# Optimization experiments

Hardware: AMD Instinct MI355X
Metric: run time of the kernel (lower is better)

Reference implementation:

```python
import jax, jax.numpy as jnp
import numpy as np

B, C, H, W = 4, 128, 64, 64


def setup_inputs() -> dict:
    key = jax.random.key(0)
    ks = jax.random.split(key, 8)
    return {
        "x": jax.random.normal(ks[0], (B, C, H, W), dtype=jnp.float32),
        "Wq": jax.random.normal(ks[1], (C // 4, C), dtype=jnp.float32) * 0.05,
        "bq": jax.random.normal(ks[2], (C // 4,), dtype=jnp.float32) * 0.05,
        "Wk": jax.random.normal(ks[3], (C // 4, C), dtype=jnp.float32) * 0.05,
        "bk": jax.random.normal(ks[4], (C // 4,), dtype=jnp.float32) * 0.05,
        "Wv": jax.random.normal(ks[5], (C, C), dtype=jnp.float32) * 0.05,
        "bv": jax.random.normal(ks[6], (C,), dtype=jnp.float32) * 0.05,
        "gamma": jnp.full((1,), 0.1, dtype=jnp.float32),
        "pos": jax.random.normal(ks[7], (1, C, 32, 32), dtype=jnp.float32) * 0.02,
    }


def reference(x, Wq, bq, Wk, bk, Wv, bv, gamma, pos):
    b, c, h, w = x.shape
    n = h * w
    # bilinear upsample of position encoding (half-pixel centers = torch align_corners=False)
    pe = jax.image.resize(pos, (1, c, h, w), method="bilinear")
    scale_factor = min(1.0, 16.0 / max(h, w))  # static shapes -> python float
    xp = x + scale_factor * 0.1 * pe
    # 1x1 conv projections as einsums; q/k: [b, c/4, n], v: [b, c, n]
    q = (jnp.einsum("bchw,oc->bohw", xp, Wq) + bq[None, :, None, None]).reshape(b, -1, n)
    k = (jnp.einsum("bchw,oc->bohw", xp, Wk) + bk[None, :, None, None]).reshape(b, -1, n)
    v = (jnp.einsum("bchw,oc->bohw", xp, Wv) + bv[None, :, None, None]).reshape(b, c, n)
    # scores[b, i, j] = <q_i, k_j> / (sqrt(C) + eps); softmax over j
    scores = jnp.einsum("bdn,bdm->bnm", q, k) / (c ** 0.5 + 1e-08)
    attn = jax.nn.softmax(scores, axis=-1)
    # out = V @ attn^T  -> [b, c, n]
    out = jnp.einsum("bcn,bmn->bcm", v, attn).reshape(b, c, h, w)
    return gamma[0] * out + xp
```

## Files before the change

kernel.cpp:

```cpp
#include <hip/hip_runtime.h>
#include <hip/hip_bf16.h>
#include <cstdint>
#include <cstddef>

typedef __attribute__((ext_vector_type(8))) short bf16x8;
typedef __attribute__((ext_vector_type(4))) float f32x4;
typedef __attribute__((ext_vector_type(16))) float f32x16;
typedef __attribute__((ext_vector_type(2))) unsigned int u32x2;
typedef unsigned int u32;
typedef unsigned short u16;
typedef unsigned char u8;

__device__ __forceinline__ u16 f2bf(float f) {
  union { float f; u32 u; } v; v.f = f;
  u32 r = v.u + 0x7FFFu + ((v.u >> 16) & 1u);
  return (u16)(r >> 16);
}
__device__ __forceinline__ u32 pk2(float a, float b) {
  return (u32)f2bf(a) | ((u32)f2bf(b) << 16);
}
__device__ __forceinline__ float bfhi(u32 u) {
  union { u32 u; float f; } v; v.u = u & 0xFFFF0000u; return v.f;
}
__device__ __forceinline__ float bflo(u32 u) {
  union { u32 u; float f; } v; v.u = u << 16; return v.f;
}
__device__ __forceinline__ float fexp2(float x) {
  return __builtin_amdgcn_exp2f(x);
}

__device__ __forceinline__ void proj_tile(int mts, int li, int g,
    const u16* tb, int tb_stride_u16, int n0, int b,
    const float* Wq, const float* bq, const float* Wk, const float* bk,
    const float* Wv, const float* bv,
    u8* q8, u8* k8, u8* v2) {
  const float qks = 0.35709468f;
  int row = mts * 16 + li;
  const float* wsrc = row < 32 ? Wq + (size_t)row * 128
                    : row < 64 ? Wk + (size_t)(row - 32) * 128
                               : Wv + (size_t)(row - 64) * 128;
  int ob = mts * 16 + g * 4;
  const float* bsrc = ob < 32 ? bq + ob : ob < 64 ? bk + (ob - 32) : bv + (ob - 64);
  f32x4 acc[4];
#pragma unroll
  for (int nt = 0; nt < 4; ++nt) acc[nt] = (f32x4){0.f, 0.f, 0.f, 0.f};
#pragma unroll
  for (int kc = 0; kc < 4; ++kc) {
    float4 wa = *(const float4*)(wsrc + kc * 32 + g * 8);
    float4 wb = *(const float4*)(wsrc + kc * 32 + g * 8 + 4);
    union { u32 u[4]; bf16x8 v; } af;
    af.u[0] = pk2(wa.x, wa.y); af.u[1] = pk2(wa.z, wa.w);
    af.u[2] = pk2(wb.x, wb.y); af.u[3] = pk2(wb.z, wb.w);
    bf16x8 bfr[4];
#pragma unroll
    for (int nt = 0; nt < 4; ++nt)
      bfr[nt] = *(const bf16x8*)(tb + (size_t)(nt * 16 + li) * tb_stride_u16 + kc * 32 + g * 8);
#pragma unroll
    for (int nt = 0; nt < 4; ++nt)
      acc[nt] = __builtin_amdgcn_mfma_f32_16x16x32_bf16(af.v, bfr[nt], acc[nt], 0, 0, 0);
  }
  float bias[4];
#pragma unroll
  for (int r = 0; r < 4; ++r) bias[r] = bsrc[r];
#pragma unroll
  for (int nt = 0; nt < 4; ++nt) {
    int n = n0 + nt * 16 + li;
    float v0 = acc[nt][0] + bias[0];
    float v1 = acc[nt][1] + bias[1];
    float v2v = acc[nt][2] + bias[2];
    float v3 = acc[nt][3] + bias[3];
    if (mts < 4) {
      v0 *= qks; v1 *= qks; v2v *= qks; v3 *= qks;
      u32 w = (u32)__builtin_amdgcn_cvt_pk_fp8_f32(v0, v1, 0, false);
      w = (u32)__builtin_amdgcn_cvt_pk_fp8_f32(v2v, v3, (int)w, true);
      u8* dst = mts < 2 ? q8 : k8;
      int obb = mts < 2 ? ob : ob - 32;
      *(u32*)(dst + (((size_t)b * 4096) + n) * 32 + obb) = w;
    } else {
      int cv = ob - 64;
      u32 w01 = (u32)__builtin_amdgcn_cvt_pk_fp8_f32(v0, v1, 0, false);
      u32 w23 = (u32)__builtin_amdgcn_cvt_pk_fp8_f32(v2v, v3, 0, false);
      size_t vb = (((size_t)b * 128 + (n >> 5)) * 128 + cv) * 32 + (n & 31);
      v2[vb]      = (u8)(w01 & 0xFF);
      v2[vb + 32] = (u8)((w01 >> 8) & 0xFF);
      v2[vb + 64] = (u8)(w23 & 0xFF);
      v2[vb + 96] = (u8)((w23 >> 8) & 0xFF);
    }
  }
}

__global__ __launch_bounds__(512) void k_pp(const float* __restrict__ x,
    const float* __restrict__ pos,
    const float* __restrict__ Wq, const float* __restrict__ bq,
    const float* __restrict__ Wk, const float* __restrict__ bk,
    const float* __restrict__ Wv, const float* __restrict__ bv,
    u8* __restrict__ q8, u8* __restrict__ k8, u8* __restrict__ v2) {
  __shared__ float tf[128][66];
  __shared__ u16 tb[64][136];
  int t = threadIdx.x;
  int n0 = blockIdx.x * 64;
  int b = blockIdx.y;
  int h = blockIdx.x;
  int hj = h >> 1;
  int ya, yb; float wa, wb;
  if ((h & 1) == 0) { ya = hj - 1 < 0 ? 0 : hj - 1; yb = hj; wa = 0.25f; wb = 0.75f; }
  else             { ya = hj; yb = hj + 1 > 31 ? 31 : hj + 1; wa = 0.75f; wb = 0.25f; }
  {
    int cl = t >> 2, q4 = t & 3;
    int w0 = q4 * 16;
    const float* pr0 = pos + (size_t)cl * 1024 + ya * 32;
    const float* pr1 = pos + (size_t)cl * 1024 + yb * 32;
    int i0 = q4 * 8;
    float rr[10];
#pragma unroll
    for (int j = 0; j < 10; ++j) {
      int idx = i0 - 1 + j;
      idx = idx < 0 ? 0 : (idx > 31 ? 31 : idx);
      rr[j] = wa * pr0[idx] + wb * pr1[idx];
    }
    size_t gbase = ((size_t)(b * 128 + cl)) * 4096 + h * 64 + w0;
#pragma unroll
    for (int u = 0; u < 4; ++u) {
      float4 xv = *(const float4*)(x + gbase + u * 4);
      float vals[4] = {xv.x, xv.y, xv.z, xv.w};
#pragma unroll
      for (int j = 0; j < 4; ++j) {
        int e = u * 4 + j;
        int li = (e >> 1) + 1;
        float pe = (e & 1) == 0 ? 0.25f * rr[li - 1] + 0.75f * rr[li]
                                : 0.75f * rr[li] + 0.25f * rr[li + 1];
        tf[cl][w0 + e] = vals[j] + 0.025f * pe;
      }
    }
  }
  __syncthreads();
  {
    int nl = t & 63, qr = t >> 6;
    u32* tbw = (u32*)&tb[0][0];
#pragma unroll
    for (int p = 0; p < 8; ++p)
      tbw[nl * 68 + qr * 8 + p] =
          pk2(tf[qr * 16 + 2 * p][nl], tf[qr * 16 + 2 * p + 1][nl]);
  }
  __syncthreads();
  int wv = t >> 6, lane = t & 63, li = lane & 15, g = lane >> 4;
  proj_tile(wv, li, g, &tb[0][0], 136, n0, b, Wq, bq, Wk, bk, Wv, bv, q8, k8, v2);
  if (wv < 4)
    proj_tile(8 + wv, li, g, &tb[0][0], 136, n0, b, Wq, bq, Wk, bk, Wv, bv, q8, k8, v2);
}

__global__ __launch_bounds__(512, 2) void k_attn(const u8* __restrict__ q8,
    const u8* __restrict__ k8, const u8* __restrict__ v2,
    const float* __restrict__ x, const float* __restrict__ pos,
    const float* __restrict__ gamma, float* __restrict__ out) {
  __shared__ u32 buf[4][32][66];
  __shared__ float ll[8][32];
  int t = threadIdx.x;
  int wv = t >> 6, lane = t & 63;
  int q = lane & 31, hi = lane >> 5;
  int flat = blockIdx.x + 64 * blockIdx.y;
  int xcd = flat & 7;
  int b = xcd >> 1;
  int qt = (xcd & 1) * 32 + (flat >> 3);
  int q0 = qt * 64;
  const u8* qb8 = q8 + (((size_t)b * 4096) + q0) * 32;
  union { uint2 u; long long l_; } qAlo, qAhi, qBlo, qBhi;
  qAlo.u = *(const uint2*)(qb8 + (size_t)q * 32 + hi * 8);
  qAhi.u = *(const uint2*)(qb8 + (size_t)q * 32 + 16 + hi * 8);
  qBlo.u = *(const uint2*)(qb8 + (size_t)(32 + q) * 32 + hi * 8);
  qBhi.u = *(const uint2*)(qb8 + (size_t)(32 + q) * 32 + 16 + hi * 8);
  f32x16 accA[4] = {}, accB[4] = {};
  const f32x16 zz = {};
  float sumA = 0.f, sumB = 0.f;
  const u8* kbb = k8 + (size_t)b * 4096 * 32;
  const u8* vbb = v2 + (size_t)b * 524288;
  int kv_beg = wv * 512;
  union { uint2 u; long long l_; } kl, kh;
  kl.u = *(const uint2*)(kbb + (size_t)(kv_beg + q) * 32 + hi * 8);
  kh.u = *(const uint2*)(kbb + (size_t)(kv_beg + q) * 32 + 16 + hi * 8);

  for (int it = 0; it < 16; ++it) {
    int kv0 = kv_beg + it * 32;
    const u8* vch = vbb + (size_t)(kv0 >> 5) * 4096 + q * 32 + hi * 8;
    uint2 vr[8];
#pragma unroll
    for (int ct = 0; ct < 4; ++ct) {
      vr[2 * ct]     = *(const uint2*)(vch + ct * 1024);
      vr[2 * ct + 1] = *(const uint2*)(vch + ct * 1024 + 16);
    }
    f32x16 sA = __builtin_amdgcn_mfma_f32_32x32x16_fp8_fp8(kl.l_, qAlo.l_, zz, 0, 0, 0);
    sA = __builtin_amdgcn_mfma_f32_32x32x16_fp8_fp8(kh.l_, qAhi.l_, sA, 0, 0, 0);
    f32x16 sB = __builtin_amdgcn_mfma_f32_32x32x16_fp8_fp8(kl.l_, qBlo.l_, zz, 0, 0, 0);
    sB = __builtin_amdgcn_mfma_f32_32x32x16_fp8_fp8(kh.l_, qBhi.l_, sB, 0, 0, 0);
    if (it < 15) {
      const u8* krn = kbb + (size_t)(kv0 + 32 + q) * 32 + hi * 8;
      kl.u = *(const uint2*)krn;
      kh.u = *(const uint2*)(krn + 16);
    }
    {
      float p[16];
#pragma unroll
      for (int r = 0; r < 16; ++r) p[r] = fexp2(sA[r]);
      float s0 = (p[0] + p[1]) + (p[2] + p[3]);
      float s1 = (p[4] + p[5]) + (p[6] + p[7]);
      float s2 = (p[8] + p[9]) + (p[10] + p[11]);
      float s3 = (p[12] + p[13]) + (p[14] + p[15]);
      sumA += (s0 + s1) + (s2 + s3);
      u32 dw0 = (u32)__builtin_amdgcn_cvt_pk_fp8_f32(p[0], p[1], 0, false);
      dw0 = (u32)__builtin_amdgcn_cvt_pk_fp8_f32(p[2], p[3], (int)dw0, true);
      u32 dw1 = (u32)__builtin_amdgcn_cvt_pk_fp8_f32(p[4], p[5], 0, false);
      dw1 = (u32)__builtin_amdgcn_cvt_pk_fp8_f32(p[6], p[7], (int)dw1, true);
      u32 dw2 = (u32)__builtin_amdgcn_cvt_pk_fp8_f32(p[8], p[9], 0, false);
      dw2 = (u32)__builtin_amdgcn_cvt_pk_fp8_f32(p[10], p[11], (int)dw2, true);
      u32 dw3 = (u32)__builtin_amdgcn_cvt_pk_fp8_f32(p[12], p[13], 0, false);
      dw3 = (u32)__builtin_amdgcn_cvt_pk_fp8_f32(p[14], p[15], (int)dw3, true);
      u32x2 sw0 = __builtin_amdgcn_permlane32_swap(dw0, dw1, false, false);
      u32x2 sw1 = __builtin_amdgcn_permlane32_swap(dw2, dw3, false, false);
      union { uint2 u; long long l_; } pf0, pf1;
      pf0.u.x = sw0[0]; pf0.u.y = sw0[1];
      pf1.u.x = sw1[0]; pf1.u.y = sw1[1];
#pragma unroll
      for (int ct = 0; ct < 4; ++ct) {
        union { uint2 u; long long l_; } v0u, v1u;
        v0u.u = vr[2 * ct]; v1u.u = vr[2 * ct + 1];
        accA[ct] = __builtin_amdgcn_mfma_f32_32x32x16_fp8_fp8(v0u.l_, pf0.l_, accA[ct], 0, 0, 0);
        accA[ct] = __builtin_amdgcn_mfma_f32_32x32x16_fp8_fp8(v1u.l_, pf1.l_, accA[ct], 0, 0, 0);
      }
    }
    {
      float p[16];
#pragma unroll
      for (int r = 0; r < 16; ++r) p[r] = fexp2(sB[r]);
      float s0 = (p[0] + p[1]) + (p[2] + p[3]);
      float s1 = (p[4] + p[5]) + (p[6] + p[7]);
      float s2 = (p[8] + p[9]) + (p[10] + p[11]);
      float s3 = (p[12] + p[13]) + (p[14] + p[15]);
      sumB += (s0 + s1) + (s2 + s3);
      u32 dw0 = (u32)__builtin_amdgcn_cvt_pk_fp8_f32(p[0], p[1], 0, false);
      dw0 = (u32)__builtin_amdgcn_cvt_pk_fp8_f32(p[2], p[3], (int)dw0, true);
      u32 dw1 = (u32)__builtin_amdgcn_cvt_pk_fp8_f32(p[4], p[5], 0, false);
      dw1 = (u32)__builtin_amdgcn_cvt_pk_fp8_f32(p[6], p[7], (int)dw1, true);
      u32 dw2 = (u32)__builtin_amdgcn_cvt_pk_fp8_f32(p[8], p[9], 0, false);
      dw2 = (u32)__builtin_amdgcn_cvt_pk_fp8_f32(p[10], p[11], (int)dw2, true);
      u32 dw3 = (u32)__builtin_amdgcn_cvt_pk_fp8_f32(p[12], p[13], 0, false);
      dw3 = (u32)__builtin_amdgcn_cvt_pk_fp8_f32(p[14], p[15], (int)dw3, true);
      u32x2 sw0 = __builtin_amdgcn_permlane32_swap(dw0, dw1, false, false);
      u32x2 sw1 = __builtin_amdgcn_permlane32_swap(dw2, dw3, false, false);
      union { uint2 u; long long l_; } pf0, pf1;
      pf0.u.x = sw0[0]; pf0.u.y = sw0[1];
      pf1.u.x = sw1[0]; pf1.u.y = sw1[1];
#pragma unroll
      for (int ct = 0; ct < 4; ++ct) {
        union { uint2 u; long long l_; } v0u, v1u;
        v0u.u = vr[2 * ct]; v1u.u = vr[2 * ct + 1];
        accB[ct] = __builtin_amdgcn_mfma_f32_32x32x16_fp8_fp8(v0u.l_, pf0.l_, accB[ct], 0, 0, 0);
        accB[ct] = __builtin_amdgcn_mfma_f32_32x32x16_fp8_fp8(v1u.l_, pf1.l_, accB[ct], 0, 0, 0);
      }
    }
  }

  float lA, lB;
  {
    union { float f; u32 u; } cv; cv.f = sumA;
    u32x2 sw = __builtin_amdgcn_permlane32_swap(cv.u, cv.u, false, false);
    union { u32 u; float f; } r0, r1; r0.u = sw[0]; r1.u = sw[1];
    lA = r0.f + r1.f;
    cv.f = sumB;
    sw = __builtin_amdgcn_permlane32_swap(cv.u, cv.u, false, false);
    r0.u = sw[0]; r1.u = sw[1];
    lB = r0.f + r1.f;
  }

  float g0 = gamma[0];
#define COMBINE_PASS(ACC, LV, QOFF)                                           \
  __syncthreads();                                                            \
  if (lane < 32) ll[wv][q] = LV;                                              \
  if (wv >= 4) {                                                              \
    int w = wv - 4;                                                           \
    _Pragma("unroll")                                                         \
    for (int ct = 0; ct < 4; ++ct)                                            \
      _Pragma("unroll")                                                       \
      for (int q4 = 0; q4 < 4; ++q4) {                                        \
        uint2 pkd;                                                            \
        pkd.x = pk2(ACC[ct][q4 * 4 + 0], ACC[ct][q4 * 4 + 1]);                \
        pkd.y = pk2(ACC[ct][q4 * 4 + 2], ACC[ct][q4 * 4 + 3]);                \
        *(uint2*)&buf[w][q][16 * ct + 4 * q4 + 2 * hi] = pkd;                 \
      }                                                                       \
  }                                                                           \
  __syncthreads();                                                            \
  if (wv < 4) {                                                               \
    float lv2 = ll[wv + 4][q];                                                \
    _Pragma("unroll")                                                         \
    for (int ct = 0; ct < 4; ++ct)                                            \
      _Pragma("unroll")                                                       \
      for (int q4 = 0; q4 < 4; ++q4) {                                        \
        uint2 pr = *(const uint2*)&buf[wv][q][16 * ct + 4 * q4 + 2 * hi];     \
        ACC[ct][q4 * 4 + 0] += bflo(pr.x);                                    \
        ACC[ct][q4 * 4 + 1] += bfhi(pr.x);                                    \
        ACC[ct][q4 * 4 + 2] += bflo(pr.y);                                    \
        ACC[ct][q4 * 4 + 3] += bfhi(pr.y);                                    \
      }                                                                       \
    _Pragma("unroll")                                                         \
    for (int ct = 0; ct < 4; ++ct)                                            \
      _Pragma("unroll")                                                       \
      for (int q4 = 0; q4 < 4; ++q4) {                                        \
        uint2 pkd;                                                            \
        pkd.x = pk2(ACC[ct][q4 * 4 + 0], ACC[ct][q4 * 4 + 1]);                \
        pkd.y = pk2(ACC[ct][q4 * 4 + 2], ACC[ct][q4 * 4 + 3]);                \
        *(uint2*)&buf[wv][q][16 * ct + 4 * q4 + 2 * hi] = pkd;                \
      }                                                                       \
    if (lane < 32) ll[wv][q] = LV + lv2;                                      \
  }                                                                           \
  __syncthreads();                                                            \
  {                                                                           \
    int qe = t & 31, cgr = t >> 5;                                            \
    float ls = ll[0][qe] + ll[1][qe] + ll[2][qe] + ll[3][qe];                 \
    float inv = 1.f / ls;                                                     \
    float sacc[8];                                                            \
    _Pragma("unroll")                                                         \
    for (int j = 0; j < 8; ++j) sacc[j] = 0.f;                                \
    _Pragma("unroll")                                                         \
    for (int w = 0; w < 4; ++w) {                                             \
      uint4 r = *(const uint4*)&buf[w][qe][cgr * 4];                          \
      sacc[0] += bflo(r.x); sacc[1] += bfhi(r.x);                             \
      sacc[2] += bflo(r.y); sacc[3] += bfhi(r.y);                             \
      sacc[4] += bflo(r.z); sacc[5] += bfhi(r.z);                             \
      sacc[6] += bflo(r.w); sacc[7] += bfhi(r.w);                             \
    }                                                                         \
    int hh = qt;                                                              \
    int hj2 = hh >> 1;                                                        \
    int ya2, ybI; float wya, wyb;                                             \
    if ((hh & 1) == 0) { ya2 = hj2 - 1 < 0 ? 0 : hj2 - 1; ybI = hj2;          \
                         wya = 0.25f; wyb = 0.75f; }                          \
    else               { ya2 = hj2; ybI = hj2 + 1 > 31 ? 31 : hj2 + 1;        \
                         wya = 0.75f; wyb = 0.25f; }                          \
    int ww = (QOFF) + qe;                                                     \
    int wj = ww >> 1;                                                         \
    int xaI, xbI; float wxa, wxb;                                             \
    if ((ww & 1) == 0) { xaI = wj - 1 < 0 ? 0 : wj - 1; xbI = wj;             \
                         wxa = 0.25f; wxb = 0.75f; }                          \
    else               { xaI = wj; xbI = wj + 1 > 31 ? 31 : wj + 1;           \
                         wxa = 0.75f; wxb = 0.25f; }                          \
    int o00 = ya2 * 32 + xaI, o01 = ya2 * 32 + xbI;                           \
    int o10 = ybI * 32 + xaI, o11 = ybI * 32 + xbI;                           \
    _Pragma("unroll")                                                         \
    for (int j = 0; j < 8; ++j) {                                             \
      int c = cgr * 8 + j;                                                    \
      const float* pj = pos + (size_t)c * 1024;                               \
      float pe = wya * (wxa * pj[o00] + wxb * pj[o01])                        \
               + wyb * (wxa * pj[o10] + wxb * pj[o11]);                       \
      size_t adr = (((size_t)b * 128) + c) * 4096 + q0 + (QOFF) + qe;         \
      out[adr] = g0 * sacc[j] * inv + x[adr] + 0.025f * pe;                   \
    }                                                                         \
  }

  COMBINE_PASS(accA, lA, 0)
  COMBINE_PASS(accB, lB, 32)
#undef COMBINE_PASS
}

extern "C" void kernel_launch(void* const* d_in, const int* in_sizes, int n_in,
                              void* d_out, int out_size, void* d_ws, size_t ws_size,
                              hipStream_t stream) {
  const float* x     = (const float*)d_in[0];
  const float* Wq    = (const float*)d_in[1];
  const float* bq    = (const float*)d_in[2];
  const float* Wk    = (const float*)d_in[3];
  const float* bk    = (const float*)d_in[4];
  const float* Wv    = (const float*)d_in[5];
  const float* bv    = (const float*)d_in[6];
  const float* gamma = (const float*)d_in[7];
  const float* pos   = (const float*)d_in[8];
  float* out = (float*)d_out;

  char* ws = (char*)d_ws;
  u8* q8 = (u8*)ws;
  u8* k8 = (u8*)(ws + 524288);
  u8* v2 = (u8*)(ws + 1048576);

  k_pp<<<dim3(64, 4), 512, 0, stream>>>(x, pos, Wq, bq, Wk, bk, Wv, bv,
                                        q8, k8, v2);
  k_attn<<<dim3(64, 4), 512, 0, stream>>>(q8, k8, v2, x, pos, gamma, out);
}
```

Measured before the change: 36.95 us.

## Halve query tile per attention block to double grid size

The attention kernel now handles 32 queries per block instead of 64, launching 512 blocks instead of 256, with launch bounds raised to 4 blocks per CU. Each block holds one accumulator set, so register pressure drops and more blocks can be resident, which should fill the GPU better and hide latency. In exchange, every K/V tile is loaded and converted twice as often across blocks, roughly doubling K/V traffic. The XCD-aware mapping and the position-encoding indexing are rewritten for the new tiling.

```diff
diff --git a/kernel.cpp b/kernel.cpp
--- a/kernel.cpp
+++ b/kernel.cpp
@@ -149,7 +149,7 @@
     proj_tile(8 + wv, li, g, &tb[0][0], 136, n0, b, Wq, bq, Wk, bk, Wv, bv, q8, k8, v2);
 }
 
-__global__ __launch_bounds__(512, 2) void k_attn(const u8* __restrict__ q8,
+__global__ __launch_bounds__(512, 4) void k_attn(const u8* __restrict__ q8,
     const u8* __restrict__ k8, const u8* __restrict__ v2,
     const float* __restrict__ x, const float* __restrict__ pos,
     const float* __restrict__ gamma, float* __restrict__ out) {
@@ -158,20 +158,18 @@
   int t = threadIdx.x;
   int wv = t >> 6, lane = t & 63;
   int q = lane & 31, hi = lane >> 5;
-  int flat = blockIdx.x + 64 * blockIdx.y;
+  int flat = blockIdx.x + 128 * blockIdx.y;
   int xcd = flat & 7;
   int b = xcd >> 1;
-  int qt = (xcd & 1) * 32 + (flat >> 3);
-  int q0 = qt * 64;
+  int qt = (xcd & 1) * 64 + (flat >> 3);
+  int q0 = qt * 32;
   const u8* qb8 = q8 + (((size_t)b * 4096) + q0) * 32;
-  union { uint2 u; long long l_; } qAlo, qAhi, qBlo, qBhi;
+  union { uint2 u; long long l_; } qAlo, qAhi;
   qAlo.u = *(const uint2*)(qb8 + (size_t)q * 32 + hi * 8);
   qAhi.u = *(const uint2*)(qb8 + (size_t)q * 32 + 16 + hi * 8);
-  qBlo.u = *(const uint2*)(qb8 + (size_t)(32 + q) * 32 + hi * 8);
-  qBhi.u = *(const uint2*)(qb8 + (size_t)(32 + q) * 32 + 16 + hi * 8);
-  f32x16 accA[4] = {}, accB[4] = {};
+  f32x16 accA[4] = {};
   const f32x16 zz = {};
-  float sumA = 0.f, sumB = 0.f;
+  float sumA = 0.f;
   const u8* kbb = k8 + (size_t)b * 4096 * 32;
   const u8* vbb = v2 + (size_t)b * 524288;
   int kv_beg = wv * 512;
@@ -190,8 +188,6 @@
     }
     f32x16 sA = __builtin_amdgcn_mfma_f32_32x32x16_fp8_fp8(kl.l_, qAlo.l_, zz, 0, 0, 0);
     sA = __builtin_amdgcn_mfma_f32_32x32x16_fp8_fp8(kh.l_, qAhi.l_, sA, 0, 0, 0);
-    f32x16 sB = __builtin_amdgcn_mfma_f32_32x32x16_fp8_fp8(kl.l_, qBlo.l_, zz, 0, 0, 0);
-    sB = __builtin_amdgcn_mfma_f32_32x32x16_fp8_fp8(kh.l_, qBhi.l_, sB, 0, 0, 0);
     if (it < 15) {
       const u8* krn = kbb + (size_t)(kv0 + 32 + q) * 32 + hi * 8;
       kl.u = *(const uint2*)krn;
@@ -227,136 +223,97 @@
         accA[ct] = __builtin_amdgcn_mfma_f32_32x32x16_fp8_fp8(v1u.l_, pf1.l_, accA[ct], 0, 0, 0);
       }
     }
-    {
-      float p[16];
-#pragma unroll
-      for (int r = 0; r < 16; ++r) p[r] = fexp2(sB[r]);
-      float s0 = (p[0] + p[1]) + (p[2] + p[3]);
-      float s1 = (p[4] + p[5]) + (p[6] + p[7]);
-      float s2 = (p[8] + p[9]) + (p[10] + p[11]);
-      float s3 = (p[12] + p[13]) + (p[14] + p[15]);
-      sumB += (s0 + s1) + (s2 + s3);
-      u32 dw0 = (u32)__builtin_amdgcn_cvt_pk_fp8_f32(p[0], p[1], 0, false);
-      dw0 = (u32)__builtin_amdgcn_cvt_pk_fp8_f32(p[2], p[3], (int)dw0, true);
-      u32 dw1 = (u32)__builtin_amdgcn_cvt_pk_fp8_f32(p[4], p[5], 0, false);
-      dw1 = (u32)__builtin_amdgcn_cvt_pk_fp8_f32(p[6], p[7], (int)dw1, true);
-      u32 dw2 = (u32)__builtin_amdgcn_cvt_pk_fp8_f32(p[8], p[9], 0, false);
-      dw2 = (u32)__builtin_amdgcn_cvt_pk_fp8_f32(p[10], p[11], (int)dw2, true);
-      u32 dw3 = (u32)__builtin_amdgcn_cvt_pk_fp8_f32(p[12], p[13], 0, false);
-      dw3 = (u32)__builtin_amdgcn_cvt_pk_fp8_f32(p[14], p[15], (int)dw3, true);
-      u32x2 sw0 = __builtin_amdgcn_permlane32_swap(dw0, dw1, false, false);
-      u32x2 sw1 = __builtin_amdgcn_permlane32_swap(dw2, dw3, false, false);
-      union { uint2 u; long long l_; } pf0, pf1;
-      pf0.u.x = sw0[0]; pf0.u.y = sw0[1];
-      pf1.u.x = sw1[0]; pf1.u.y = sw1[1];
-#pragma unroll
-      for (int ct = 0; ct < 4; ++ct) {
-        union { uint2 u; long long l_; } v0u, v1u;
-        v0u.u = vr[2 * ct]; v1u.u = vr[2 * ct + 1];
-        accB[ct] = __builtin_amdgcn_mfma_f32_32x32x16_fp8_fp8(v0u.l_, pf0.l_, accB[ct], 0, 0, 0);
-        accB[ct] = __builtin_amdgcn_mfma_f32_32x32x16_fp8_fp8(v1u.l_, pf1.l_, accB[ct], 0, 0, 0);
-      }
-    }
-  }
-
-  float lA, lB;
+  }
+
+  float lA;
   {
     union { float f; u32 u; } cv; cv.f = sumA;
     u32x2 sw = __builtin_amdgcn_permlane32_swap(cv.u, cv.u, false, false);
     union { u32 u; float f; } r0, r1; r0.u = sw[0]; r1.u = sw[1];
     lA = r0.f + r1.f;
-    cv.f = sumB;
-    sw = __builtin_amdgcn_permlane32_swap(cv.u, cv.u, false, false);
-    r0.u = sw[0]; r1.u = sw[1];
-    lB = r0.f + r1.f;
   }
 
   float g0 = gamma[0];
-#define COMBINE_PASS(ACC, LV, QOFF)                                           \
-  __syncthreads();                                                            \
-  if (lane < 32) ll[wv][q] = LV;                                              \
-  if (wv >= 4) {                                                              \
-    int w = wv - 4;                                                           \
-    _Pragma("unroll")                                                         \
-    for (int ct = 0; ct < 4; ++ct)                                            \
-      _Pragma("unroll")                                                       \
-      for (int q4 = 0; q4 < 4; ++q4) {                                        \
-        uint2 pkd;                                                            \
-        pkd.x = pk2(ACC[ct][q4 * 4 + 0], ACC[ct][q4 * 4 + 1]);                \
-        pkd.y = pk2(ACC[ct][q4 * 4 + 2], ACC[ct][q4 * 4 + 3]);                \
-        *(uint2*)&buf[w][q][16 * ct + 4 * q4 + 2 * hi] = pkd;                 \
-      }                                                                       \
-  }                                                                           \
-  __syncthreads();                                                            \
-  if (wv < 4) {                                                               \
-    float lv2 = ll[wv + 4][q];                                                \
-    _Pragma("unroll")                                                         \
-    for (int ct = 0; ct < 4; ++ct)                                            \
-      _Pragma("unroll")                                                       \
-      for (int q4 = 0; q4 < 4; ++q4) {                                        \
-        uint2 pr = *(const uint2*)&buf[wv][q][16 * ct + 4 * q4 + 2 * hi];     \
-        ACC[ct][q4 * 4 + 0] += bflo(pr.x);                                    \
-        ACC[ct][q4 * 4 + 1] += bfhi(pr.x);                                    \
-        ACC[ct][q4 * 4 + 2] += bflo(pr.y);                                    \
-        ACC[ct][q4 * 4 + 3] += bfhi(pr.y);                                    \
-      }                                                                       \
-    _Pragma("unroll")                                                         \
-    for (int ct = 0; ct < 4; ++ct)                                            \
-      _Pragma("unroll")                                                       \
-      for (int q4 = 0; q4 < 4; ++q4) {                                        \
-        uint2 pkd;                                                            \
-        pkd.x = pk2(ACC[ct][q4 * 4 + 0], ACC[ct][q4 * 4 + 1]);                \
-        pkd.y = pk2(ACC[ct][q4 * 4 + 2], ACC[ct][q4 * 4 + 3]);                \
-        *(uint2*)&buf[wv][q][16 * ct + 4 * q4 + 2 * hi] = pkd;                \
-      }                                                                       \
-    if (lane < 32) ll[wv][q] = LV + lv2;                                      \
-  }                                                                           \
-  __syncthreads();                                                            \
-  {                                                                           \
-    int qe = t & 31, cgr = t >> 5;                                            \
-    float ls = ll[0][qe] + ll[1][qe] + ll[2][qe] + ll[3][qe];                 \
-    float inv = 1.f / ls;                                                     \
-    float sacc[8];                                                            \
-    _Pragma("unroll")                                                         \
-    for (int j = 0; j < 8; ++j) sacc[j] = 0.f;                                \
-    _Pragma("unroll")                                                         \
-    for (int w = 0; w < 4; ++w) {                                             \
-      uint4 r = *(const uint4*)&buf[w][qe][cgr * 4];                          \
-      sacc[0] += bflo(r.x); sacc[1] += bfhi(r.x);                             \
-      sacc[2] += bflo(r.y); sacc[3] += bfhi(r.y);                             \
-      sacc[4] += bflo(r.z); sacc[5] += bfhi(r.z);                             \
-      sacc[6] += bflo(r.w); sacc[7] += bfhi(r.w);                             \
-    }                                                                         \
-    int hh = qt;                                                              \
-    int hj2 = hh >> 1;                                                        \
-    int ya2, ybI; float wya, wyb;                                             \
-    if ((hh & 1) == 0) { ya2 = hj2 - 1 < 0 ? 0 : hj2 - 1; ybI = hj2;          \
-                         wya = 0.25f; wyb = 0.75f; }                          \
-    else               { ya2 = hj2; ybI = hj2 + 1 > 31 ? 31 : hj2 + 1;        \
-                         wya = 0.75f; wyb = 0.25f; }                          \
-    int ww = (QOFF) + qe;                                                     \
-    int wj = ww >> 1;                                                         \
-    int xaI, xbI; float wxa, wxb;                                             \
-    if ((ww & 1) == 0) { xaI = wj - 1 < 0 ? 0 : wj - 1; xbI = wj;             \
-                         wxa = 0.25f; wxb = 0.75f; }                          \
-    else               { xaI = wj; xbI = wj + 1 > 31 ? 31 : wj + 1;           \
-                         wxa = 0.75f; wxb = 0.25f; }                          \
-    int o00 = ya2 * 32 + xaI, o01 = ya2 * 32 + xbI;                           \
-    int o10 = ybI * 32 + xaI, o11 = ybI * 32 + xbI;                           \
-    _Pragma("unroll")                                                         \
-    for (int j = 0; j < 8; ++j) {                                             \
-      int c = cgr * 8 + j;                                                    \
-      const float* pj = pos + (size_t)c * 1024;                               \
-      float pe = wya * (wxa * pj[o00] + wxb * pj[o01])                        \
-               + wyb * (wxa * pj[o10] + wxb * pj[o11]);                       \
-      size_t adr = (((size_t)b * 128) + c) * 4096 + q0 + (QOFF) + qe;         \
-      out[adr] = g0 * sacc[j] * inv + x[adr] + 0.025f * pe;                   \
-    }                                                                         \
-  }
-
-  COMBINE_PASS(accA, lA, 0)
-  COMBINE_PASS(accB, lB, 32)
-#undef COMBINE_PASS
+  __syncthreads();
+  if (lane < 32) ll[wv][q] = lA;
+  if (wv >= 4) {
+    int w = wv - 4;
+#pragma unroll
+    for (int ct = 0; ct < 4; ++ct)
+#pragma unroll
+      for (int q4 = 0; q4 < 4; ++q4) {
+        uint2 pkd;
+        pkd.x = pk2(accA[ct][q4 * 4 + 0], accA[ct][q4 * 4 + 1]);
+        pkd.y = pk2(accA[ct][q4 * 4 + 2], accA[ct][q4 * 4 + 3]);
+        *(uint2*)&buf[w][q][16 * ct + 4 * q4 + 2 * hi] = pkd;
+      }
+  }
+  __syncthreads();
+  if (wv < 4) {
+    float lv2 = ll[wv + 4][q];
+#pragma unroll
+    for (int ct = 0; ct < 4; ++ct)
+#pragma unroll
+      for (int q4 = 0; q4 < 4; ++q4) {
+        uint2 pr = *(const uint2*)&buf[wv][q][16 * ct + 4 * q4 + 2 * hi];
+        accA[ct][q4 * 4 + 0] += bflo(pr.x);
+        accA[ct][q4 * 4 + 1] += bfhi(pr.x);
+        accA[ct][q4 * 4 + 2] += bflo(pr.y);
+        accA[ct][q4 * 4 + 3] += bfhi(pr.y);
+      }
+#pragma unroll
+    for (int ct = 0; ct < 4; ++ct)
+#pragma unroll
+      for (int q4 = 0; q4 < 4; ++q4) {
+        uint2 pkd;
+        pkd.x = pk2(accA[ct][q4 * 4 + 0], accA[ct][q4 * 4 + 1]);
+        pkd.y = pk2(accA[ct][q4 * 4 + 2], accA[ct][q4 * 4 + 3]);
+        *(uint2*)&buf[wv][q][16 * ct + 4 * q4 + 2 * hi] = pkd;
+      }
+    if (lane < 32) ll[wv][q] = lA + lv2;
+  }
+  __syncthreads();
+  {
+    int qe = t & 31, cgr = t >> 5;
+    float ls = ll[0][qe] + ll[1][qe] + ll[2][qe] + ll[3][qe];
+    float inv = 1.f / ls;
+    float sacc[8];
+#pragma unroll
+    for (int j = 0; j < 8; ++j) sacc[j] = 0.f;
+#pragma unroll
+    for (int w = 0; w < 4; ++w) {
+      uint4 r = *(const uint4*)&buf[w][qe][cgr * 4];
+      sacc[0] += bflo(r.x); sacc[1] += bfhi(r.x);
+      sacc[2] += bflo(r.y); sacc[3] += bfhi(r.y);
+      sacc[4] += bflo(r.z); sacc[5] += bfhi(r.z);
+      sacc[6] += bflo(r.w); sacc[7] += bfhi(r.w);
+    }
+    int hh = qt >> 1;
+    int hj2 = hh >> 1;
+    int ya2, ybI; float wya, wyb;
+    if ((hh & 1) == 0) { ya2 = hj2 - 1 < 0 ? 0 : hj2 - 1; ybI = hj2;
+                         wya = 0.25f; wyb = 0.75f; }
+    else               { ya2 = hj2; ybI = hj2 + 1 > 31 ? 31 : hj2 + 1;
+                         wya = 0.75f; wyb = 0.25f; }
+    int ww = (qt & 1) * 32 + qe;
+    int wj = ww >> 1;
+    int xaI, xbI; float wxa, wxb;
+    if ((ww & 1) == 0) { xaI = wj - 1 < 0 ? 0 : wj - 1; xbI = wj;
+                         wxa = 0.25f; wxb = 0.75f; }
+    else               { xaI = wj; xbI = wj + 1 > 31 ? 31 : wj + 1;
+                         wxa = 0.75f; wxb = 0.25f; }
+    int o00 = ya2 * 32 + xaI, o01 = ya2 * 32 + xbI;
+    int o10 = ybI * 32 + xaI, o11 = ybI * 32 + xbI;
+#pragma unroll
+    for (int j = 0; j < 8; ++j) {
+      int c = cgr * 8 + j;
+      const float* pj = pos + (size_t)c * 1024;
+      float pe = wya * (wxa * pj[o00] + wxb * pj[o01])
+               + wyb * (wxa * pj[o10] + wxb * pj[o11]);
+      size_t adr = (((size_t)b * 128) + c) * 4096 + q0 + qe;
+      out[adr] = g0 * sacc[j] * inv + x[adr] + 0.025f * pe;
+    }
+  }
 }
 
 extern "C" void kernel_launch(void* const* d_in, const int* in_sizes, int n_in,
@@ -380,5 +337,5 @@
 
   k_pp<<<dim3(64, 4), 512, 0, stream>>>(x, pos, Wq, bq, Wk, bk, Wv, bv,
                                         q8, k8, v2);
-  k_attn<<<dim3(64, 4), 512, 0, stream>>>(q8, k8, v2, x, pos, gamma, out);
-}
+  k_attn<<<dim3(128, 4), 512, 0, stream>>>(q8, k8, v2, x, pos, gamma, out);
+}
```

Result: slower. 41.69 us (+12.8%).
